# Kernel optimization log

Measured on AMD Instinct MI355X. Metric: run time of the kernel, lower is better.

The kernel has to match this reference:

```python
import jax, jax.numpy as jnp
import numpy as np

B, N, D, K, H = 4, 128, 256, 128, 32
A, E = 128, 512  # num_atoms, num_edges (edge types)


def _nonlinear(x, W1, b1, W2, b2):
    # torch NonLinear: Linear -> exact GELU -> Linear
    return jax.nn.gelu(x @ W1 + b1, approximate=False) @ W2 + b2


def setup_inputs() -> dict:
    key = jax.random.key(0)
    ks = jax.random.split(key, 32)
    pos = jax.random.normal(ks[0], (B, N, 3), dtype=jnp.float32) * 3.0
    x = jax.random.randint(ks[1], (B, N, 9), 1, A + 1)          # avoid padding idx 0
    node_type_edge = jax.random.randint(ks[2], (B, N, N, 2), 1, E)
    # 9 atom embedding tables, padding_idx=0 rows zeroed
    atom_emb = (jax.random.normal(ks[3], (9, A + 1, D), dtype=jnp.float32) * 0.02).at[:, 0].set(0.0)
    sc = D ** -0.5
    W_la = jax.random.normal(ks[4], (D, D), dtype=jnp.float32) * sc
    W_ra = jax.random.normal(ks[5], (D, D), dtype=jnp.float32) * sc
    W_ld = jax.random.normal(ks[6], (D, D), dtype=jnp.float32) * sc
    W_rd = jax.random.normal(ks[7], (D, D), dtype=jnp.float32) * sc
    gbf_means = jax.random.normal(ks[8], (K,), dtype=jnp.float32)
    gbf_stds = jax.random.uniform(ks[9], (K,), dtype=jnp.float32, minval=0.5, maxval=3.0)
    src_mul = (jax.random.normal(ks[10], (E,), dtype=jnp.float32) * 0.1).at[0].set(0.0)
    tgt_mul = (jax.random.normal(ks[11], (E,), dtype=jnp.float32) * 0.1).at[0].set(0.0)
    src_bias = (jax.random.normal(ks[12], (E,), dtype=jnp.float32) * 0.1).at[0].set(0.0)
    tgt_bias = (jax.random.normal(ks[13], (E,), dtype=jnp.float32) * 0.1).at[0].set(0.0)
    gbf_W1 = jax.random.normal(ks[14], (K, K), dtype=jnp.float32) * (K ** -0.5)
    gbf_b1 = jnp.zeros((K,), jnp.float32)
    gbf_W2 = jax.random.normal(ks[15], (K, H), dtype=jnp.float32) * (K ** -0.5)
    gbf_b2 = jnp.zeros((H,), jnp.float32)
    dih_W1 = jax.random.normal(ks[16], (D, D), dtype=jnp.float32) * sc
    dih_b1 = jnp.zeros((D,), jnp.float32)
    dih_W2 = jax.random.normal(ks[17], (D, H), dtype=jnp.float32) * sc
    dih_b2 = jnp.zeros((H,), jnp.float32)
    ang_W1 = jax.random.normal(ks[18], (D, D), dtype=jnp.float32) * sc
    ang_b1 = jnp.zeros((D,), jnp.float32)
    ang_W2 = jax.random.normal(ks[19], (D, D), dtype=jnp.float32) * sc
    ang_b2 = jnp.zeros((D,), jnp.float32)
    return dict(pos=pos, atom_emb=atom_emb, W_la=W_la, W_ra=W_ra, W_ld=W_ld, W_rd=W_rd,
                gbf_means=gbf_means, gbf_stds=gbf_stds, src_mul=src_mul, tgt_mul=tgt_mul,
                src_bias=src_bias, tgt_bias=tgt_bias, gbf_W1=gbf_W1, gbf_b1=gbf_b1,
                gbf_W2=gbf_W2, gbf_b2=gbf_b2, dih_W1=dih_W1, dih_b1=dih_b1, dih_W2=dih_W2,
                dih_b2=dih_b2, ang_W1=ang_W1, ang_b1=ang_b1, ang_W2=ang_W2, ang_b2=ang_b2,
                x=x, node_type_edge=node_type_edge)


def _forward(pos, atom_emb, W_la, W_ra, W_ld, W_rd, gbf_means, gbf_stds,
             src_mul, tgt_mul, src_bias, tgt_bias, gbf_W1, gbf_b1, gbf_W2, gbf_b2,
             dih_W1, dih_b1, dih_W2, dih_b2, ang_W1, ang_b1, ang_W2, ang_b2,
             x, node_type_edge):
    no_pos = (~jnp.all(pos == 0, axis=(-1, -2))).astype(pos.dtype)  # [B]
    # sum of 9 per-feature embeddings  -> [B, N, D]
    node_feature = sum(atom_emb[i][x[..., i]] for i in range(9))
    padding_mask = jnp.all(x == 0, axis=-1)                         # [B, N]
    # delta_pos[b,i,j] = pos[b,j] - pos[b,i]
    delta_pos = pos[:, None, :, :] - pos[:, :, None, :]             # [B, N, N, 3]
    dist = jnp.linalg.norm(delta_pos, axis=-1)                      # [B, N, N]
    delta_pos = delta_pos / (dist[..., None] + 1e-5)
    # node_vec_feature[b,i,c,d] = node_feature[b,i,d] * sum_j (1-pad_j) delta_pos[b,i,j,c]
    # (exact fusion of edge_vec_feature -> masked sum, since node_feature only depends on i)
    keep = (~padding_mask).astype(pos.dtype)                        # [B, N]
    s = jnp.einsum('bijc,bj->bic', delta_pos, keep)                 # [B, N, 3]
    node_vec = node_feature[:, :, None, :] * s[..., None]           # [B, N, 3, D]
    # angle feature
    angle = jnp.sum((node_vec @ W_la) * (node_vec @ W_ra), axis=-2)  # [B, N, D]
    angle = _nonlinear(angle, ang_W1, ang_b1, ang_W2, ang_b2)
    angle = angle * no_pos[:, None, None]
    # gaussian RPE
    et = node_type_edge
    mul = src_mul[et[..., 0]] + tgt_mul[et[..., 1]]                 # [B, N, N]
    bias = src_bias[et[..., 0]] + tgt_bias[et[..., 1]]
    xg = mul[..., None] * dist[..., None] + bias[..., None]         # [B, N, N, 1] -> K
    std = jnp.abs(gbf_stds) + 0.01
    a = (2.0 * 3.14159) ** 0.5
    edge_feature = jnp.exp(-0.5 * ((xg - gbf_means) / std) ** 2) / (a * std)  # [B,N,N,K]
    gbf_result = _nonlinear(edge_feature, gbf_W1, gbf_b1, gbf_W2, gbf_b2)     # [B,N,N,H]
    # dihedral: vector rejection of projected node vec features onto edge directions
    left = node_vec @ W_ld                                          # [B, N, 3, D]
    right = node_vec @ W_rd
    Ld = jnp.einsum('bjcd,bijc->bijd', left, delta_pos)             # proj of left (indexed j)
    wl = left[:, None] - Ld[..., None, :] * delta_pos[..., None]    # [B, N, N, 3, D]
    Rd = jnp.einsum('bicd,bijc->bijd', right, -delta_pos)           # proj of right (indexed i)
    wr = right[:, :, None] - Rd[..., None, :] * (-delta_pos)[..., None]
    edge_dih = jnp.sum(wl * wr, axis=-2)                            # [B, N, N, D]
    edge_dih = _nonlinear(edge_dih, dih_W1, dih_b1, dih_W2, dih_b2)  # [B, N, N, H]
    attn_bias = (gbf_result + edge_dih) * no_pos[:, None, None, None]
    attn_bias = jnp.transpose(attn_bias, (0, 3, 1, 2))              # [B, H, N, N]
    attn_bias = jnp.where(padding_mask[:, None, None, :], -jnp.inf, attn_bias)
    return attn_bias, angle, delta_pos


def reference(pos, atom_emb, W_la, W_ra, W_ld, W_rd, gbf_means, gbf_stds,
              src_mul, tgt_mul, src_bias, tgt_bias, gbf_W1, gbf_b1, gbf_W2, gbf_b2,
              dih_W1, dih_b1, dih_W2, dih_b2, ang_W1, ang_b1, ang_W2, ang_b2,
              x, node_type_edge):
    return _forward(pos, atom_emb, W_la, W_ra, W_ld, W_rd, gbf_means, gbf_stds,
                    src_mul, tgt_mul, src_bias, tgt_bias, gbf_W1, gbf_b1, gbf_W2, gbf_b2,
                    dih_W1, dih_b1, dih_W2, dih_b2, ang_W1, ang_b1, ang_W2, ang_b2,
                    x, node_type_edge)
```

## Files before the change

kernel.cpp:

```cpp
#include <hip/hip_runtime.h>
#include <math.h>

#define BB 4
#define NN 128
#define DD 256
#define KK 128
#define HH 32
#define AA 128
#define EE 512

typedef float f32x4 __attribute__((ext_vector_type(4)));
typedef short short8 __attribute__((ext_vector_type(8)));
typedef unsigned short ushort4v __attribute__((ext_vector_type(4)));

__device__ __forceinline__ float gelu_fast(float x) {
    float x2 = x * x;
    float t = x * fmaf(x2, 0.0713548162726f, 1.59576912161f);
    float e = __expf(-t);
    return x * __builtin_amdgcn_rcpf(1.0f + e);
}

__device__ __forceinline__ unsigned short f2bf(float f) {
    unsigned int u = __float_as_uint(f);
    u = u + 0x7fffu + ((u >> 16) & 1u);
    return (unsigned short)(u >> 16);
}

__device__ __forceinline__ int swz512(int row, int colByte) {
    return row * 512 + (colByte ^ ((row & 7) << 4));
}
__device__ __forceinline__ int swz256(int row, int colByte) {
    return row * 256 + (colByte ^ ((row & 7) << 4));
}

__global__ void k1_geom(const float* __restrict__ pos, const int* __restrict__ x,
                        float* __restrict__ out_dp, float* __restrict__ dist_ws,
                        float* __restrict__ s_ws, float* __restrict__ keep,
                        float* __restrict__ no_pos) {
    int bi = blockIdx.x;
    int b = bi >> 7;
    int i = bi & 127;
    int j = threadIdx.x;
    int bj = b * NN + j;

    int allz = 1;
    #pragma unroll
    for (int f = 0; f < 9; ++f) allz &= (x[bj * 9 + f] == 0);
    float kj = allz ? 0.0f : 1.0f;

    __shared__ int flag;
    if (j == 0) flag = 0;

    float pix = pos[bi * 3 + 0], piy = pos[bi * 3 + 1], piz = pos[bi * 3 + 2];
    float pjx = pos[bj * 3 + 0], pjy = pos[bj * 3 + 1], pjz = pos[bj * 3 + 2];
    float dx = pjx - pix, dy = pjy - piy, dz = pjz - piz;
    float dist = sqrtf(dx * dx + dy * dy + dz * dz);
    float inv = 1.0f / (dist + 1e-5f);
    dx *= inv; dy *= inv; dz *= inv;
    size_t e = (size_t)bi * NN + j;
    out_dp[e * 3 + 0] = dx;
    out_dp[e * 3 + 1] = dy;
    out_dp[e * 3 + 2] = dz;
    dist_ws[e] = dist;

    __shared__ float red[3][128];
    red[0][j] = kj * dx; red[1][j] = kj * dy; red[2][j] = kj * dz;
    __syncthreads();
    if (pjx != 0.0f || pjy != 0.0f || pjz != 0.0f) flag = 1;
    for (int off = 64; off > 0; off >>= 1) {
        if (j < off) {
            red[0][j] += red[0][j + off];
            red[1][j] += red[1][j + off];
            red[2][j] += red[2][j + off];
        }
        __syncthreads();
    }
    if (j == 0) {
        s_ws[bi * 3 + 0] = red[0][0];
        s_ws[bi * 3 + 1] = red[1][0];
        s_ws[bi * 3 + 2] = red[2][0];
    }
    if (i == 0) {
        keep[bj] = kj;
        if (j == 0) no_pos[b] = flag ? 1.0f : 0.0f;
    }
}

__global__ __launch_bounds__(256) void k_nf(const float* __restrict__ atom_emb,
                                            const int* __restrict__ x,
                                            unsigned short* __restrict__ nf_ws) {
    int bn = blockIdx.x;
    int t = threadIdx.x;
    float acc = 0.0f;
    #pragma unroll
    for (int f = 0; f < 9; ++f) {
        int xi = x[bn * 9 + f];
        acc += atom_emb[((size_t)(f * (AA + 1) + xi)) * DD + t];
    }
    nf_ws[(size_t)bn * DD + t] = f2bf(acc);
}

__global__ void k_pack(const float* __restrict__ dW1, const float* __restrict__ dW2,
                       const float* __restrict__ gW1, const float* __restrict__ gW2,
                       const float* __restrict__ wla, const float* __restrict__ wra,
                       const float* __restrict__ wld, const float* __restrict__ wrd,
                       const float* __restrict__ aW1, const float* __restrict__ aW2,
                       unsigned short* __restrict__ out) {
    int idx = blockIdx.x * 256 + threadIdx.x;
    const float* W; int Nc, base, k, c8;
    if (idx < 8192)       { W = dW1; Nc = 256; base = 0;     int li = idx;         k = li >> 5; c8 = li & 31; }
    else if (idx < 9216)  { W = dW2; Nc = 32;  base = 65536; int li = idx - 8192;  k = li >> 2; c8 = li & 3; }
    else if (idx < 11264) { W = gW1; Nc = 128; base = 73728; int li = idx - 9216;  k = li >> 4; c8 = li & 15; }
    else if (idx < 11776) { W = gW2; Nc = 32;  base = 90112; int li = idx - 11264; k = li >> 2; c8 = li & 3; }
    else if (idx < 60928) {
        int q  = (idx - 11776) >> 13;
        int li = (idx - 11776) & 8191;
        W = (q == 0) ? wla : (q == 1) ? wra : (q == 2) ? wld : (q == 3) ? wrd : (q == 4) ? aW1 : aW2;
        Nc = 256; base = 94208 + q * 65536; k = li >> 5; c8 = li & 31;
    }
    else return;
    int ntiles = Nc >> 4;
    int ks = k >> 5, hi = (k & 31) >> 3, ee = k & 7;
    const float* wp = &W[k * Nc + c8 * 8];
    float4 a = *reinterpret_cast<const float4*>(wp);
    float4 b4 = *reinterpret_cast<const float4*>(wp + 4);
    float vals[8] = {a.x, a.y, a.z, a.w, b4.x, b4.y, b4.z, b4.w};
    #pragma unroll
    for (int jj = 0; jj < 8; ++jj) {
        int c = c8 * 8 + jj;
        int nt = c >> 4, lo = c & 15;
        out[base + (((ks * ntiles + nt) * 64) + hi * 16 + lo) * 8 + ee] = f2bf(vals[jj]);
    }
}

__device__ __forceinline__ void stage32x256(const unsigned short* __restrict__ src, int bn0,
                                            unsigned short* sA, int t) {
    #pragma unroll
    for (int r = 0; r < 4; ++r) {
        int idx = r * 256 + t;
        int row = idx >> 5;
        int c8 = idx & 31;
        short8 v = *reinterpret_cast<const short8*>(&src[((size_t)(bn0 + row)) * DD + c8 * 8]);
        *reinterpret_cast<short8*>((char*)sA + swz512(row, c8 * 16)) = v;
    }
}

__device__ __forceinline__ void gemm_nt(const unsigned short* __restrict__ Bp, int nt,
                                        const unsigned short* sA, int l, int lo, int hi,
                                        f32x4 acc[2]) {
    for (int ks = 0; ks < 8; ++ks) {
        short8 a0 = *reinterpret_cast<const short8*>((const char*)sA + swz512(lo, ks * 64 + hi * 16));
        short8 a1 = *reinterpret_cast<const short8*>((const char*)sA + swz512(16 + lo, ks * 64 + hi * 16));
        short8 bfr = *reinterpret_cast<const short8*>(&Bp[(((size_t)ks * 16 + nt) * 64 + l) * 8]);
        acc[0] = __builtin_amdgcn_mfma_f32_16x16x32_bf16(a0, bfr, acc[0], 0, 0, 0);
        acc[1] = __builtin_amdgcn_mfma_f32_16x16x32_bf16(a1, bfr, acc[1], 0, 0, 0);
    }
}

__global__ __launch_bounds__(256, 4) void k2a(
    const unsigned short* __restrict__ nf_ws,
    const unsigned short* __restrict__ Wla_p, const unsigned short* __restrict__ Wra_p,
    const unsigned short* __restrict__ Wld_p, const unsigned short* __restrict__ Wrd_p,
    const float* __restrict__ s_ws,
    float* __restrict__ ld_ws, float* __restrict__ rd_ws,
    unsigned short* __restrict__ ap_ws) {
    int blk = blockIdx.x;
    int c = blk & 3, tile = blk >> 2;
    int bn0 = tile * 32;
    int t = threadIdx.x;
    int w = t >> 6, l = t & 63, lo = l & 15, hi = l >> 4;
    int nt = c * 4 + w;

    __shared__ __align__(16) unsigned short sA[32 * 256];
    __shared__ float ls2[32];
    if (t < 32) {
        float a0 = s_ws[(bn0 + t) * 3 + 0];
        float a1 = s_ws[(bn0 + t) * 3 + 1];
        float a2 = s_ws[(bn0 + t) * 3 + 2];
        ls2[t] = a0 * a0 + a1 * a1 + a2 * a2;
    }
    stage32x256(nf_ws, bn0, sA, t);
    __syncthreads();

    f32x4 a_la[2] = {}, a_ra[2] = {}, a_ld[2] = {}, a_rd[2] = {};
    gemm_nt(Wla_p, nt, sA, l, lo, hi, a_la);
    gemm_nt(Wra_p, nt, sA, l, lo, hi, a_ra);
    gemm_nt(Wld_p, nt, sA, l, lo, hi, a_ld);
    gemm_nt(Wrd_p, nt, sA, l, lo, hi, a_rd);

    int col = nt * 16 + lo;
    #pragma unroll
    for (int m = 0; m < 2; ++m) {
        #pragma unroll
        for (int r = 0; r < 4; ++r) {
            int row = m * 16 + hi * 4 + r;
            size_t off = (size_t)(bn0 + row) * DD + col;
            ld_ws[off] = a_ld[m][r];
            rd_ws[off] = a_rd[m][r];
            ap_ws[off] = f2bf(ls2[row] * a_la[m][r] * a_ra[m][r]);
        }
    }
}

__global__ __launch_bounds__(256, 4) void k2b(
    const unsigned short* __restrict__ ap_ws, const unsigned short* __restrict__ WaW1_p,
    const float* __restrict__ ang_b1, unsigned short* __restrict__ hid_ws) {
    int blk = blockIdx.x;
    int c = blk & 3, tile = blk >> 2;
    int bn0 = tile * 32;
    int t = threadIdx.x;
    int w = t >> 6, l = t & 63, lo = l & 15, hi = l >> 4;
    int nt = c * 4 + w;

    __shared__ __align__(16) unsigned short sA[32 * 256];
    stage32x256(ap_ws, bn0, sA, t);
    __syncthreads();

    f32x4 acc[2] = {};
    gemm_nt(WaW1_p, nt, sA, l, lo, hi, acc);

    int col = nt * 16 + lo;
    float b1v = ang_b1[col];
    #pragma unroll
    for (int m = 0; m < 2; ++m)
        #pragma unroll
        for (int r = 0; r < 4; ++r)
            hid_ws[(size_t)(bn0 + m * 16 + hi * 4 + r) * DD + col] = f2bf(gelu_fast(acc[m][r] + b1v));
}

__global__ __launch_bounds__(256, 4) void k2c(
    const unsigned short* __restrict__ hid_ws, const unsigned short* __restrict__ WaW2_p,
    const float* __restrict__ ang_b2, const float* __restrict__ no_pos,
    float* __restrict__ out_angle) {
    int blk = blockIdx.x;
    int c = blk & 3, tile = blk >> 2;
    int bn0 = tile * 32;
    int t = threadIdx.x;
    int w = t >> 6, l = t & 63, lo = l & 15, hi = l >> 4;
    int nt = c * 4 + w;

    __shared__ __align__(16) unsigned short sA[32 * 256];
    stage32x256(hid_ws, bn0, sA, t);
    __syncthreads();

    f32x4 acc[2] = {};
    gemm_nt(WaW2_p, nt, sA, l, lo, hi, acc);

    int col = nt * 16 + lo;
    float b2v = ang_b2[col];
    float lnp = no_pos[tile >> 2];
    #pragma unroll
    for (int m = 0; m < 2; ++m)
        #pragma unroll
        for (int r = 0; r < 4; ++r)
            out_angle[(size_t)(bn0 + m * 16 + hi * 4 + r) * DD + col] = (acc[m][r] + b2v) * lnp;
}

__global__ __launch_bounds__(256, 2) void k3_mfma(
    const unsigned short* __restrict__ Wp1, const unsigned short* __restrict__ Wp2,
    const unsigned short* __restrict__ Wg1, const unsigned short* __restrict__ Wg2,
    const float* __restrict__ dih_b1, const float* __restrict__ dih_b2,
    const float* __restrict__ gbf_b1, const float* __restrict__ gbf_b2,
    const float* __restrict__ gbf_means, const float* __restrict__ gbf_stds,
    const float* __restrict__ src_mul, const float* __restrict__ tgt_mul,
    const float* __restrict__ src_bias, const float* __restrict__ tgt_bias,
    const int* __restrict__ nte,
    const float* __restrict__ ld_ws, const float* __restrict__ rd_ws,
    const float* __restrict__ s_ws, const float* __restrict__ dist_ws,
    const float* __restrict__ keep, const float* __restrict__ no_pos,
    const float* __restrict__ dp_in,
    float* __restrict__ out_attn) {
    int blk = blockIdx.x;
    int jh = blk & 1;
    int i  = (blk >> 1) & 127;
    int b  = blk >> 8;
    int j0 = jh * 64;
    int t = threadIdx.x;
    int w  = t >> 6;
    int l  = t & 63;
    int lo = l & 15;
    int hi = l >> 4;

    __shared__ __align__(16) unsigned short sE[64 * 256];
    __shared__ __align__(16) unsigned short sH[64 * 256];
    __shared__ __align__(16) float rd_l[DD];
    __shared__ float sg[64], sxg[64], skeep[64];
    __shared__ __align__(16) float lmean[KK], linv[KK], lcoef[KK];

    int bi = b * NN + i;

    if (t < 64) {
        int j = j0 + t;
        size_t e = (size_t)bi * NN + j;
        float d0 = dp_in[e * 3 + 0], d1 = dp_in[e * 3 + 1], d2 = dp_in[e * 3 + 2];
        float si0 = s_ws[bi * 3 + 0], si1 = s_ws[bi * 3 + 1], si2 = s_ws[bi * 3 + 2];
        int bj = b * NN + j;
        float sj0 = s_ws[bj * 3 + 0], sj1 = s_ws[bj * 3 + 1], sj2 = s_ws[bj * 3 + 2];
        float u = sj0 * d0 + sj1 * d1 + sj2 * d2;
        float v = si0 * d0 + si1 * d1 + si2 * d2;
        float dp2 = d0 * d0 + d1 * d1 + d2 * d2;
        sg[t] = (si0 * sj0 + si1 * sj1 + si2 * sj2) - u * v * (2.0f - dp2);
        int et0 = nte[e * 2 + 0], et1 = nte[e * 2 + 1];
        sxg[t] = (src_mul[et0] + tgt_mul[et1]) * dist_ws[e] + src_bias[et0] + tgt_bias[et1];
        skeep[t] = keep[bj];
    } else if (t < 128) {
        int q = t - 64;
        reinterpret_cast<float4*>(rd_l)[q] =
            reinterpret_cast<const float4*>(&rd_ws[(size_t)bi * DD])[q];
    } else {
        int k = t - 128;
        float s = fabsf(gbf_stds[k]) + 0.01f;
        lmean[k] = gbf_means[k];
        linv[k] = 1.0f / s;
        lcoef[k] = 1.0f / (2.5066262f * s);
    }
    __syncthreads();

    {
        const float* ldbase = &ld_ws[((size_t)(b * NN + j0)) * DD];
        #pragma unroll
        for (int r = 0; r < 8; ++r) {
            int idx = r * 256 + t;
            int row = idx >> 5;
            int c8  = idx & 31;
            float g = sg[row];
            const float* lp = ldbase + row * DD + c8 * 8;
            float4 l0 = *reinterpret_cast<const float4*>(lp);
            float4 l1 = *reinterpret_cast<const float4*>(lp + 4);
            float4 r0 = *reinterpret_cast<const float4*>(&rd_l[c8 * 8]);
            float4 r1 = *reinterpret_cast<const float4*>(&rd_l[c8 * 8 + 4]);
            short8 vv;
            vv[0] = (short)f2bf(g * l0.x * r0.x);
            vv[1] = (short)f2bf(g * l0.y * r0.y);
            vv[2] = (short)f2bf(g * l0.z * r0.z);
            vv[3] = (short)f2bf(g * l0.w * r0.w);
            vv[4] = (short)f2bf(g * l1.x * r1.x);
            vv[5] = (short)f2bf(g * l1.y * r1.y);
            vv[6] = (short)f2bf(g * l1.z * r1.z);
            vv[7] = (short)f2bf(g * l1.w * r1.w);
            *reinterpret_cast<short8*>((char*)sE + swz512(row, c8 * 16)) = vv;
        }
        unsigned short* sG = sH;
        #pragma unroll
        for (int r = 0; r < 4; ++r) {
            int idx = r * 256 + t;
            int row = idx >> 4;
            int c8  = idx & 15;
            float xv = sxg[row];
            float4 m0 = *reinterpret_cast<const float4*>(&lmean[c8 * 8]);
            float4 m1 = *reinterpret_cast<const float4*>(&lmean[c8 * 8 + 4]);
            float4 i0 = *reinterpret_cast<const float4*>(&linv[c8 * 8]);
            float4 i1 = *reinterpret_cast<const float4*>(&linv[c8 * 8 + 4]);
            float4 c0 = *reinterpret_cast<const float4*>(&lcoef[c8 * 8]);
            float4 c1 = *reinterpret_cast<const float4*>(&lcoef[c8 * 8 + 4]);
            float z;
            short8 vv;
            z = (xv - m0.x) * i0.x; vv[0] = (short)f2bf(c0.x * __expf(-0.5f * z * z));
            z = (xv - m0.y) * i0.y; vv[1] = (short)f2bf(c0.y * __expf(-0.5f * z * z));
            z = (xv - m0.z) * i0.z; vv[2] = (short)f2bf(c0.z * __expf(-0.5f * z * z));
            z = (xv - m0.w) * i0.w; vv[3] = (short)f2bf(c0.w * __expf(-0.5f * z * z));
            z = (xv - m1.x) * i1.x; vv[4] = (short)f2bf(c1.x * __expf(-0.5f * z * z));
            z = (xv - m1.y) * i1.y; vv[5] = (short)f2bf(c1.y * __expf(-0.5f * z * z));
            z = (xv - m1.z) * i1.z; vv[6] = (short)f2bf(c1.z * __expf(-0.5f * z * z));
            z = (xv - m1.w) * i1.w; vv[7] = (short)f2bf(c1.w * __expf(-0.5f * z * z));
            *reinterpret_cast<short8*>((char*)sG + swz256(row, c8 * 16)) = vv;
        }
    }
    __syncthreads();

    f32x4 accg[4][2] = {};
    {
        const unsigned short* sG = sH;
        for (int ks = 0; ks < 4; ++ks) {
            short8 a[4];
            #pragma unroll
            for (int m = 0; m < 4; ++m)
                a[m] = *reinterpret_cast<const short8*>((const char*)sG + swz256(m * 16 + lo, ks * 64 + hi * 16));
            #pragma unroll
            for (int n = 0; n < 2; ++n) {
                short8 bfr = *reinterpret_cast<const short8*>(&Wg1[(((size_t)ks * 8 + (w * 2 + n)) * 64 + l) * 8]);
                #pragma unroll
                for (int m = 0; m < 4; ++m)
                    accg[m][n] = __builtin_amdgcn_mfma_f32_16x16x32_bf16(a[m], bfr, accg[m][n], 0, 0, 0);
            }
        }
    }
    f32x4 acc[4][4] = {};
    for (int ks = 0; ks < 8; ++ks) {
        short8 a[4];
        #pragma unroll
        for (int m = 0; m < 4; ++m)
            a[m] = *reinterpret_cast<const short8*>((const char*)sE + swz512(m * 16 + lo, ks * 64 + hi * 16));
        #pragma unroll
        for (int n = 0; n < 4; ++n) {
            short8 bfr = *reinterpret_cast<const short8*>(&Wp1[(((size_t)ks * 16 + (w * 4 + n)) * 64 + l) * 8]);
            #pragma unroll
            for (int m = 0; m < 4; ++m)
                acc[m][n] = __builtin_amdgcn_mfma_f32_16x16x32_bf16(a[m], bfr, acc[m][n], 0, 0, 0);
        }
    }
    __syncthreads();

    {
        #pragma unroll
        for (int n = 0; n < 4; ++n) {
            int col = w * 64 + n * 16 + lo;
            float b1v = dih_b1[col];
            #pragma unroll
            for (int m = 0; m < 4; ++m) {
                int row0 = m * 16 + hi * 4;
                #pragma unroll
                for (int r = 0; r < 4; ++r) {
                    *reinterpret_cast<unsigned short*>((char*)sH + swz512(row0 + r, col * 2)) =
                        f2bf(gelu_fast(acc[m][n][r] + b1v));
                }
            }
        }
        unsigned short* sGH = sE;
        #pragma unroll
        for (int n = 0; n < 2; ++n) {
            int col = w * 32 + n * 16 + lo;
            float b1v = gbf_b1[col];
            #pragma unroll
            for (int m = 0; m < 4; ++m) {
                int row0 = m * 16 + hi * 4;
                #pragma unroll
                for (int r = 0; r < 4; ++r) {
                    *reinterpret_cast<unsigned short*>((char*)sGH + swz256(row0 + r, col * 2)) =
                        f2bf(gelu_fast(accg[m][n][r] + b1v));
                }
            }
        }
    }
    __syncthreads();

    f32x4 acc2d[2] = {};
    for (int ks = 0; ks < 8; ++ks) {
        short8 a = *reinterpret_cast<const short8*>((const char*)sH + swz512(w * 16 + lo, ks * 64 + hi * 16));
        #pragma unroll
        for (int n = 0; n < 2; ++n) {
            short8 bfr = *reinterpret_cast<const short8*>(&Wp2[(((size_t)ks * 2 + n) * 64 + l) * 8]);
            acc2d[n] = __builtin_amdgcn_mfma_f32_16x16x32_bf16(a, bfr, acc2d[n], 0, 0, 0);
        }
    }
    f32x4 acc2g[2] = {};
    {
        const unsigned short* sGH = sE;
        for (int ks = 0; ks < 4; ++ks) {
            short8 a = *reinterpret_cast<const short8*>((const char*)sGH + swz256(w * 16 + lo, ks * 64 + hi * 16));
            #pragma unroll
            for (int n = 0; n < 2; ++n) {
                short8 bfr = *reinterpret_cast<const short8*>(&Wg2[(((size_t)ks * 2 + n) * 64 + l) * 8]);
                acc2g[n] = __builtin_amdgcn_mfma_f32_16x16x32_bf16(a, bfr, acc2g[n], 0, 0, 0);
            }
        }
    }

    float npos = no_pos[b];
    int e0 = w * 16 + hi * 4;
    #pragma unroll
    for (int n = 0; n < 2; ++n) {
        int h = n * 16 + lo;
        float bsum = dih_b2[h] + gbf_b2[h];
        float4 v;
        float vr;
        vr = (acc2d[n][0] + acc2g[n][0] + bsum) * npos; v.x = (skeep[e0 + 0] == 0.0f) ? -INFINITY : vr;
        vr = (acc2d[n][1] + acc2g[n][1] + bsum) * npos; v.y = (skeep[e0 + 1] == 0.0f) ? -INFINITY : vr;
        vr = (acc2d[n][2] + acc2g[n][2] + bsum) * npos; v.z = (skeep[e0 + 2] == 0.0f) ? -INFINITY : vr;
        vr = (acc2d[n][3] + acc2g[n][3] + bsum) * npos; v.w = (skeep[e0 + 3] == 0.0f) ? -INFINITY : vr;
        *reinterpret_cast<float4*>(&out_attn[(((size_t)b * HH + h) * NN + i) * NN + j0 + e0]) = v;
    }
}

extern "C" void kernel_launch(void* const* d_in, const int* in_sizes, int n_in,
                              void* d_out, int out_size, void* d_ws, size_t ws_size,
                              hipStream_t stream) {
    const float* pos       = (const float*)d_in[0];
    const float* atom_emb  = (const float*)d_in[1];
    const float* W_la      = (const float*)d_in[2];
    const float* W_ra      = (const float*)d_in[3];
    const float* W_ld      = (const float*)d_in[4];
    const float* W_rd      = (const float*)d_in[5];
    const float* gbf_means = (const float*)d_in[6];
    const float* gbf_stds  = (const float*)d_in[7];
    const float* src_mul   = (const float*)d_in[8];
    const float* tgt_mul   = (const float*)d_in[9];
    const float* src_bias  = (const float*)d_in[10];
    const float* tgt_bias  = (const float*)d_in[11];
    const float* gbf_W1    = (const float*)d_in[12];
    const float* gbf_b1    = (const float*)d_in[13];
    const float* gbf_W2    = (const float*)d_in[14];
    const float* gbf_b2    = (const float*)d_in[15];
    const float* dih_W1    = (const float*)d_in[16];
    const float* dih_b1    = (const float*)d_in[17];
    const float* dih_W2    = (const float*)d_in[18];
    const float* dih_b2    = (const float*)d_in[19];
    const float* ang_W1    = (const float*)d_in[20];
    const float* ang_b1    = (const float*)d_in[21];
    const float* ang_W2    = (const float*)d_in[22];
    const float* ang_b2    = (const float*)d_in[23];
    const int*   x         = (const int*)d_in[24];
    const int*   nte       = (const int*)d_in[25];

    float* out = (float*)d_out;
    float* out_attn  = out;
    float* out_angle = out + (size_t)BB * HH * NN * NN;
    float* out_dp    = out_angle + (size_t)BB * NN * DD;

    float* ws = (float*)d_ws;
    float* keep    = ws;
    float* no_pos  = ws + 512;
    float* s_ws    = ws + 1024;
    float* dist_ws = ws + 4096;
    float* ld_ws   = ws + 4096 + 65536;
    float* rd_ws   = ld_ws + (size_t)BB * NN * DD;
    unsigned short* wp = (unsigned short*)(ws + 331776);
    unsigned short* Wp1    = wp;
    unsigned short* Wp2    = wp + 65536;
    unsigned short* Wg1    = wp + 73728;
    unsigned short* Wg2    = wp + 90112;
    unsigned short* Wla_p  = wp + 94208;
    unsigned short* Wra_p  = wp + 159744;
    unsigned short* Wld_p  = wp + 225280;
    unsigned short* Wrd_p  = wp + 290816;
    unsigned short* WaW1_p = wp + 356352;
    unsigned short* WaW2_p = wp + 421888;
    unsigned short* nf_ws  = (unsigned short*)(ws + 575488);
    unsigned short* ap_ws  = (unsigned short*)(ws + 641024);
    unsigned short* hid_ws = (unsigned short*)(ws + 706560);

    k1_geom<<<dim3(BB * NN), dim3(NN), 0, stream>>>(pos, x, out_dp, dist_ws, s_ws, keep, no_pos);
    k_nf<<<dim3(BB * NN), dim3(256), 0, stream>>>(atom_emb, x, nf_ws);
    k_pack<<<dim3(238), dim3(256), 0, stream>>>(dih_W1, dih_W2, gbf_W1, gbf_W2,
                                                W_la, W_ra, W_ld, W_rd, ang_W1, ang_W2, wp);
    k2a<<<dim3(64), dim3(256), 0, stream>>>(nf_ws, Wla_p, Wra_p, Wld_p, Wrd_p,
                                            s_ws, ld_ws, rd_ws, ap_ws);
    k2b<<<dim3(64), dim3(256), 0, stream>>>(ap_ws, WaW1_p, ang_b1, hid_ws);
    k2c<<<dim3(64), dim3(256), 0, stream>>>(hid_ws, WaW2_p, ang_b2, no_pos, out_angle);
    k3_mfma<<<dim3(BB * NN * 2), dim3(256), 0, stream>>>(
        Wp1, Wp2, Wg1, Wg2, dih_b1, dih_b2, gbf_b1, gbf_b2,
        gbf_means, gbf_stds, src_mul, tgt_mul, src_bias, tgt_bias, nte,
        ld_ws, rd_ws, s_ws, dist_ws, keep, no_pos, out_dp, out_attn);
}
```

Measured before the change: 157.7 us.

## Merge setup kernels and fold angle MLP into main attention kernel

Combines the geometry, node-feature, and weight-packing kernels into one launch that dispatches on block index. The two angle MLP GEMM kernels are also folded into the main attention-bias kernel as 16 extra blocks, with the hidden activations kept in shared memory instead of a global workspace. This removes several kernel launches and a global round trip for the hidden tensor. In exchange, the geometry blocks leave half their threads idle, and the angle blocks now do more work each and share the main kernel's register and LDS footprint.

```diff
diff --git a/kernel.cpp b/kernel.cpp
--- a/kernel.cpp
+++ b/kernel.cpp
@@ -11,7 +11,6 @@
 
 typedef float f32x4 __attribute__((ext_vector_type(4)));
 typedef short short8 __attribute__((ext_vector_type(8)));
-typedef unsigned short ushort4v __attribute__((ext_vector_type(4)));
 
 __device__ __forceinline__ float gelu_fast(float x) {
     float x2 = x * x;
@@ -33,103 +32,111 @@
     return row * 256 + (colByte ^ ((row & 7) << 4));
 }
 
-__global__ void k1_geom(const float* __restrict__ pos, const int* __restrict__ x,
-                        float* __restrict__ out_dp, float* __restrict__ dist_ws,
-                        float* __restrict__ s_ws, float* __restrict__ keep,
-                        float* __restrict__ no_pos) {
-    int bi = blockIdx.x;
-    int b = bi >> 7;
-    int i = bi & 127;
-    int j = threadIdx.x;
-    int bj = b * NN + j;
-
-    int allz = 1;
-    #pragma unroll
-    for (int f = 0; f < 9; ++f) allz &= (x[bj * 9 + f] == 0);
-    float kj = allz ? 0.0f : 1.0f;
-
-    __shared__ int flag;
-    if (j == 0) flag = 0;
-
-    float pix = pos[bi * 3 + 0], piy = pos[bi * 3 + 1], piz = pos[bi * 3 + 2];
-    float pjx = pos[bj * 3 + 0], pjy = pos[bj * 3 + 1], pjz = pos[bj * 3 + 2];
-    float dx = pjx - pix, dy = pjy - piy, dz = pjz - piz;
-    float dist = sqrtf(dx * dx + dy * dy + dz * dz);
-    float inv = 1.0f / (dist + 1e-5f);
-    dx *= inv; dy *= inv; dz *= inv;
-    size_t e = (size_t)bi * NN + j;
-    out_dp[e * 3 + 0] = dx;
-    out_dp[e * 3 + 1] = dy;
-    out_dp[e * 3 + 2] = dz;
-    dist_ws[e] = dist;
-
-    __shared__ float red[3][128];
-    red[0][j] = kj * dx; red[1][j] = kj * dy; red[2][j] = kj * dz;
-    __syncthreads();
-    if (pjx != 0.0f || pjy != 0.0f || pjz != 0.0f) flag = 1;
-    for (int off = 64; off > 0; off >>= 1) {
-        if (j < off) {
-            red[0][j] += red[0][j + off];
-            red[1][j] += red[1][j + off];
-            red[2][j] += red[2][j + off];
+__global__ __launch_bounds__(256) void k_setup(
+    const float* __restrict__ pos, const int* __restrict__ x,
+    const float* __restrict__ atom_emb,
+    const float* __restrict__ dW1, const float* __restrict__ dW2,
+    const float* __restrict__ gW1, const float* __restrict__ gW2,
+    const float* __restrict__ wla, const float* __restrict__ wra,
+    const float* __restrict__ wld, const float* __restrict__ wrd,
+    const float* __restrict__ aW1, const float* __restrict__ aW2,
+    float* __restrict__ out_dp, float* __restrict__ dist_ws,
+    float* __restrict__ s_ws, float* __restrict__ keep, float* __restrict__ no_pos,
+    unsigned short* __restrict__ nf_ws, unsigned short* __restrict__ wpack) {
+    int blk = blockIdx.x;
+    int t = threadIdx.x;
+
+    if (blk < 512) {
+        int bi = blk;
+        int b = bi >> 7;
+        int i = bi & 127;
+        __shared__ float red[3][128];
+        __shared__ int flag;
+        if (t == 0) flag = 0;
+        float kj = 0.0f, dx = 0.0f, dy = 0.0f, dz = 0.0f;
+        float pjx = 0.0f, pjy = 0.0f, pjz = 0.0f;
+        int bj = b * NN + (t & 127);
+        if (t < 128) {
+            int j = t;
+            int allz = 1;
+            #pragma unroll
+            for (int f = 0; f < 9; ++f) allz &= (x[bj * 9 + f] == 0);
+            kj = allz ? 0.0f : 1.0f;
+            float pix = pos[bi * 3 + 0], piy = pos[bi * 3 + 1], piz = pos[bi * 3 + 2];
+            pjx = pos[bj * 3 + 0]; pjy = pos[bj * 3 + 1]; pjz = pos[bj * 3 + 2];
+            dx = pjx - pix; dy = pjy - piy; dz = pjz - piz;
+            float dist = sqrtf(dx * dx + dy * dy + dz * dz);
+            float inv = 1.0f / (dist + 1e-5f);
+            dx *= inv; dy *= inv; dz *= inv;
+            size_t e = (size_t)bi * NN + j;
+            out_dp[e * 3 + 0] = dx;
+            out_dp[e * 3 + 1] = dy;
+            out_dp[e * 3 + 2] = dz;
+            dist_ws[e] = dist;
+            red[0][j] = kj * dx; red[1][j] = kj * dy; red[2][j] = kj * dz;
         }
         __syncthreads();
-    }
-    if (j == 0) {
-        s_ws[bi * 3 + 0] = red[0][0];
-        s_ws[bi * 3 + 1] = red[1][0];
-        s_ws[bi * 3 + 2] = red[2][0];
-    }
-    if (i == 0) {
-        keep[bj] = kj;
-        if (j == 0) no_pos[b] = flag ? 1.0f : 0.0f;
-    }
-}
-
-__global__ __launch_bounds__(256) void k_nf(const float* __restrict__ atom_emb,
-                                            const int* __restrict__ x,
-                                            unsigned short* __restrict__ nf_ws) {
-    int bn = blockIdx.x;
-    int t = threadIdx.x;
-    float acc = 0.0f;
-    #pragma unroll
-    for (int f = 0; f < 9; ++f) {
-        int xi = x[bn * 9 + f];
-        acc += atom_emb[((size_t)(f * (AA + 1) + xi)) * DD + t];
-    }
-    nf_ws[(size_t)bn * DD + t] = f2bf(acc);
-}
-
-__global__ void k_pack(const float* __restrict__ dW1, const float* __restrict__ dW2,
-                       const float* __restrict__ gW1, const float* __restrict__ gW2,
-                       const float* __restrict__ wla, const float* __restrict__ wra,
-                       const float* __restrict__ wld, const float* __restrict__ wrd,
-                       const float* __restrict__ aW1, const float* __restrict__ aW2,
-                       unsigned short* __restrict__ out) {
-    int idx = blockIdx.x * 256 + threadIdx.x;
-    const float* W; int Nc, base, k, c8;
-    if (idx < 8192)       { W = dW1; Nc = 256; base = 0;     int li = idx;         k = li >> 5; c8 = li & 31; }
-    else if (idx < 9216)  { W = dW2; Nc = 32;  base = 65536; int li = idx - 8192;  k = li >> 2; c8 = li & 3; }
-    else if (idx < 11264) { W = gW1; Nc = 128; base = 73728; int li = idx - 9216;  k = li >> 4; c8 = li & 15; }
-    else if (idx < 11776) { W = gW2; Nc = 32;  base = 90112; int li = idx - 11264; k = li >> 2; c8 = li & 3; }
-    else if (idx < 60928) {
-        int q  = (idx - 11776) >> 13;
-        int li = (idx - 11776) & 8191;
-        W = (q == 0) ? wla : (q == 1) ? wra : (q == 2) ? wld : (q == 3) ? wrd : (q == 4) ? aW1 : aW2;
-        Nc = 256; base = 94208 + q * 65536; k = li >> 5; c8 = li & 31;
-    }
-    else return;
-    int ntiles = Nc >> 4;
-    int ks = k >> 5, hi = (k & 31) >> 3, ee = k & 7;
-    const float* wp = &W[k * Nc + c8 * 8];
-    float4 a = *reinterpret_cast<const float4*>(wp);
-    float4 b4 = *reinterpret_cast<const float4*>(wp + 4);
-    float vals[8] = {a.x, a.y, a.z, a.w, b4.x, b4.y, b4.z, b4.w};
-    #pragma unroll
-    for (int jj = 0; jj < 8; ++jj) {
-        int c = c8 * 8 + jj;
-        int nt = c >> 4, lo = c & 15;
-        out[base + (((ks * ntiles + nt) * 64) + hi * 16 + lo) * 8 + ee] = f2bf(vals[jj]);
+        if (t < 128) {
+            if (pjx != 0.0f || pjy != 0.0f || pjz != 0.0f) flag = 1;
+        }
+        for (int off = 64; off > 0; off >>= 1) {
+            if (t < off) {
+                red[0][t] += red[0][t + off];
+                red[1][t] += red[1][t + off];
+                red[2][t] += red[2][t + off];
+            }
+            __syncthreads();
+        }
+        if (t == 0) {
+            s_ws[bi * 3 + 0] = red[0][0];
+            s_ws[bi * 3 + 1] = red[1][0];
+            s_ws[bi * 3 + 2] = red[2][0];
+        }
+        if (i == 0 && t < 128) {
+            keep[bj] = kj;
+            if (t == 0) no_pos[b] = flag ? 1.0f : 0.0f;
+        }
+        return;
+    }
+
+    if (blk < 1024) {
+        int bn = blk - 512;
+        float acc = 0.0f;
+        #pragma unroll
+        for (int f = 0; f < 9; ++f) {
+            int xi = x[bn * 9 + f];
+            acc += atom_emb[((size_t)(f * (AA + 1) + xi)) * DD + t];
+        }
+        nf_ws[(size_t)bn * DD + t] = f2bf(acc);
+        return;
+    }
+
+    {
+        int idx = (blk - 1024) * 256 + t;
+        const float* W; int Nc, base, k, c8;
+        if (idx < 8192)       { W = dW1; Nc = 256; base = 0;     int li = idx;         k = li >> 5; c8 = li & 31; }
+        else if (idx < 9216)  { W = dW2; Nc = 32;  base = 65536; int li = idx - 8192;  k = li >> 2; c8 = li & 3; }
+        else if (idx < 11264) { W = gW1; Nc = 128; base = 73728; int li = idx - 9216;  k = li >> 4; c8 = li & 15; }
+        else if (idx < 11776) { W = gW2; Nc = 32;  base = 90112; int li = idx - 11264; k = li >> 2; c8 = li & 3; }
+        else if (idx < 60928) {
+            int q  = (idx - 11776) >> 13;
+            int li = (idx - 11776) & 8191;
+            W = (q == 0) ? wla : (q == 1) ? wra : (q == 2) ? wld : (q == 3) ? wrd : (q == 4) ? aW1 : aW2;
+            Nc = 256; base = 94208 + q * 65536; k = li >> 5; c8 = li & 31;
+        }
+        else return;
+        int ntiles = Nc >> 4;
+        int ks = k >> 5, hi = (k & 31) >> 3, ee = k & 7;
+        const float* wp = &W[k * Nc + c8 * 8];
+        float4 a = *reinterpret_cast<const float4*>(wp);
+        float4 b4 = *reinterpret_cast<const float4*>(wp + 4);
+        float vals[8] = {a.x, a.y, a.z, a.w, b4.x, b4.y, b4.z, b4.w};
+        #pragma unroll
+        for (int jj = 0; jj < 8; ++jj) {
+            int c = c8 * 8 + jj;
+            int nt = c >> 4, lo = c & 15;
+            wpack[base + (((ks * ntiles + nt) * 64) + hi * 16 + lo) * 8 + ee] = f2bf(vals[jj]);
+        }
     }
 }
 
@@ -154,6 +161,25 @@
         short8 bfr = *reinterpret_cast<const short8*>(&Bp[(((size_t)ks * 16 + nt) * 64 + l) * 8]);
         acc[0] = __builtin_amdgcn_mfma_f32_16x16x32_bf16(a0, bfr, acc[0], 0, 0, 0);
         acc[1] = __builtin_amdgcn_mfma_f32_16x16x32_bf16(a1, bfr, acc[1], 0, 0, 0);
+    }
+}
+
+__device__ __forceinline__ void gemm_chunk32(const unsigned short* __restrict__ Bp,
+                                             const unsigned short* sAp,
+                                             int w, int l, int lo, int hi,
+                                             f32x4 acc[2][4]) {
+    for (int ks = 0; ks < 8; ++ks) {
+        short8 a[2];
+        #pragma unroll
+        for (int m = 0; m < 2; ++m)
+            a[m] = *reinterpret_cast<const short8*>((const char*)sAp + swz512(m * 16 + lo, ks * 64 + hi * 16));
+        #pragma unroll
+        for (int n = 0; n < 4; ++n) {
+            short8 bfr = *reinterpret_cast<const short8*>(&Bp[(((size_t)ks * 16 + (w * 4 + n)) * 64 + l) * 8]);
+            #pragma unroll
+            for (int m = 0; m < 2; ++m)
+                acc[m][n] = __builtin_amdgcn_mfma_f32_16x16x32_bf16(a[m], bfr, acc[m][n], 0, 0, 0);
+        }
     }
 }
 
@@ -202,79 +228,23 @@
     }
 }
 
-__global__ __launch_bounds__(256, 4) void k2b(
-    const unsigned short* __restrict__ ap_ws, const unsigned short* __restrict__ WaW1_p,
-    const float* __restrict__ ang_b1, unsigned short* __restrict__ hid_ws) {
-    int blk = blockIdx.x;
-    int c = blk & 3, tile = blk >> 2;
-    int bn0 = tile * 32;
-    int t = threadIdx.x;
-    int w = t >> 6, l = t & 63, lo = l & 15, hi = l >> 4;
-    int nt = c * 4 + w;
-
-    __shared__ __align__(16) unsigned short sA[32 * 256];
-    stage32x256(ap_ws, bn0, sA, t);
-    __syncthreads();
-
-    f32x4 acc[2] = {};
-    gemm_nt(WaW1_p, nt, sA, l, lo, hi, acc);
-
-    int col = nt * 16 + lo;
-    float b1v = ang_b1[col];
-    #pragma unroll
-    for (int m = 0; m < 2; ++m)
-        #pragma unroll
-        for (int r = 0; r < 4; ++r)
-            hid_ws[(size_t)(bn0 + m * 16 + hi * 4 + r) * DD + col] = f2bf(gelu_fast(acc[m][r] + b1v));
-}
-
-__global__ __launch_bounds__(256, 4) void k2c(
-    const unsigned short* __restrict__ hid_ws, const unsigned short* __restrict__ WaW2_p,
-    const float* __restrict__ ang_b2, const float* __restrict__ no_pos,
-    float* __restrict__ out_angle) {
-    int blk = blockIdx.x;
-    int c = blk & 3, tile = blk >> 2;
-    int bn0 = tile * 32;
-    int t = threadIdx.x;
-    int w = t >> 6, l = t & 63, lo = l & 15, hi = l >> 4;
-    int nt = c * 4 + w;
-
-    __shared__ __align__(16) unsigned short sA[32 * 256];
-    stage32x256(hid_ws, bn0, sA, t);
-    __syncthreads();
-
-    f32x4 acc[2] = {};
-    gemm_nt(WaW2_p, nt, sA, l, lo, hi, acc);
-
-    int col = nt * 16 + lo;
-    float b2v = ang_b2[col];
-    float lnp = no_pos[tile >> 2];
-    #pragma unroll
-    for (int m = 0; m < 2; ++m)
-        #pragma unroll
-        for (int r = 0; r < 4; ++r)
-            out_angle[(size_t)(bn0 + m * 16 + hi * 4 + r) * DD + col] = (acc[m][r] + b2v) * lnp;
-}
-
-__global__ __launch_bounds__(256, 2) void k3_mfma(
+__global__ __launch_bounds__(256, 2) void k_mega(
     const unsigned short* __restrict__ Wp1, const unsigned short* __restrict__ Wp2,
     const unsigned short* __restrict__ Wg1, const unsigned short* __restrict__ Wg2,
+    const unsigned short* __restrict__ WaW1_p, const unsigned short* __restrict__ WaW2_p,
     const float* __restrict__ dih_b1, const float* __restrict__ dih_b2,
     const float* __restrict__ gbf_b1, const float* __restrict__ gbf_b2,
+    const float* __restrict__ ang_b1, const float* __restrict__ ang_b2,
     const float* __restrict__ gbf_means, const float* __restrict__ gbf_stds,
     const float* __restrict__ src_mul, const float* __restrict__ tgt_mul,
     const float* __restrict__ src_bias, const float* __restrict__ tgt_bias,
     const int* __restrict__ nte,
+    const unsigned short* __restrict__ ap_ws,
     const float* __restrict__ ld_ws, const float* __restrict__ rd_ws,
     const float* __restrict__ s_ws, const float* __restrict__ dist_ws,
     const float* __restrict__ keep, const float* __restrict__ no_pos,
     const float* __restrict__ dp_in,
-    float* __restrict__ out_attn) {
-    int blk = blockIdx.x;
-    int jh = blk & 1;
-    int i  = (blk >> 1) & 127;
-    int b  = blk >> 8;
-    int j0 = jh * 64;
+    float* __restrict__ out_angle, float* __restrict__ out_attn) {
     int t = threadIdx.x;
     int w  = t >> 6;
     int l  = t & 63;
@@ -286,6 +256,55 @@
     __shared__ __align__(16) float rd_l[DD];
     __shared__ float sg[64], sxg[64], skeep[64];
     __shared__ __align__(16) float lmean[KK], linv[KK], lcoef[KK];
+
+    if (blockIdx.x < 16) {
+        int tile = blockIdx.x;
+        int bn0 = tile * 32;
+        stage32x256(ap_ws, bn0, sE, t);
+        __syncthreads();
+        {
+            f32x4 acc[2][4] = {};
+            gemm_chunk32(WaW1_p, sE, w, l, lo, hi, acc);
+            #pragma unroll
+            for (int n = 0; n < 4; ++n) {
+                int col = w * 64 + n * 16 + lo;
+                float b1v = ang_b1[col];
+                #pragma unroll
+                for (int m = 0; m < 2; ++m)
+                    #pragma unroll
+                    for (int r = 0; r < 4; ++r) {
+                        int row = m * 16 + hi * 4 + r;
+                        *reinterpret_cast<unsigned short*>((char*)sH + swz512(row, col * 2)) =
+                            f2bf(gelu_fast(acc[m][n][r] + b1v));
+                    }
+            }
+        }
+        __syncthreads();
+        {
+            f32x4 acc[2][4] = {};
+            gemm_chunk32(WaW2_p, sH, w, l, lo, hi, acc);
+            float lnp = no_pos[tile >> 2];
+            #pragma unroll
+            for (int n = 0; n < 4; ++n) {
+                int col = w * 64 + n * 16 + lo;
+                float b2v = ang_b2[col];
+                #pragma unroll
+                for (int m = 0; m < 2; ++m)
+                    #pragma unroll
+                    for (int r = 0; r < 4; ++r) {
+                        int row = m * 16 + hi * 4 + r;
+                        out_angle[(size_t)(bn0 + row) * DD + col] = (acc[m][n][r] + b2v) * lnp;
+                    }
+            }
+        }
+        return;
+    }
+
+    int blk = blockIdx.x - 16;
+    int jh = blk & 1;
+    int i  = (blk >> 1) & 127;
+    int b  = blk >> 8;
+    int j0 = jh * 64;
 
     int bi = b * NN + i;
 
@@ -527,18 +546,17 @@
     unsigned short* WaW2_p = wp + 421888;
     unsigned short* nf_ws  = (unsigned short*)(ws + 575488);
     unsigned short* ap_ws  = (unsigned short*)(ws + 641024);
-    unsigned short* hid_ws = (unsigned short*)(ws + 706560);
-
-    k1_geom<<<dim3(BB * NN), dim3(NN), 0, stream>>>(pos, x, out_dp, dist_ws, s_ws, keep, no_pos);
-    k_nf<<<dim3(BB * NN), dim3(256), 0, stream>>>(atom_emb, x, nf_ws);
-    k_pack<<<dim3(238), dim3(256), 0, stream>>>(dih_W1, dih_W2, gbf_W1, gbf_W2,
-                                                W_la, W_ra, W_ld, W_rd, ang_W1, ang_W2, wp);
+
+    k_setup<<<dim3(1262), dim3(256), 0, stream>>>(
+        pos, x, atom_emb, dih_W1, dih_W2, gbf_W1, gbf_W2,
+        W_la, W_ra, W_ld, W_rd, ang_W1, ang_W2,
+        out_dp, dist_ws, s_ws, keep, no_pos, nf_ws, wp);
     k2a<<<dim3(64), dim3(256), 0, stream>>>(nf_ws, Wla_p, Wra_p, Wld_p, Wrd_p,
                                             s_ws, ld_ws, rd_ws, ap_ws);
-    k2b<<<dim3(64), dim3(256), 0, stream>>>(ap_ws, WaW1_p, ang_b1, hid_ws);
-    k2c<<<dim3(64), dim3(256), 0, stream>>>(hid_ws, WaW2_p, ang_b2, no_pos, out_angle);
-    k3_mfma<<<dim3(BB * NN * 2), dim3(256), 0, stream>>>(
-        Wp1, Wp2, Wg1, Wg2, dih_b1, dih_b2, gbf_b1, gbf_b2,
+    k_mega<<<dim3(16 + BB * NN * 2), dim3(256), 0, stream>>>(
+        Wp1, Wp2, Wg1, Wg2, WaW1_p, WaW2_p,
+        dih_b1, dih_b2, gbf_b1, gbf_b2, ang_b1, ang_b2,
         gbf_means, gbf_stds, src_mul, tgt_mul, src_bias, tgt_bias, nte,
-        ld_ws, rd_ws, s_ws, dist_ws, keep, no_pos, out_dp, out_attn);
-}
+        ap_ws, ld_ws, rd_ws, s_ws, dist_ws, keep, no_pos, out_dp,
+        out_angle, out_attn);
+}
```

Result: faster. 149.5 us (-5.2%).
